# Kernel tuning notes

Measured on AMD Instinct MI355X. Metric: run time of the kernel, lower is better.

The kernel has to match this reference:

```python
import jax, jax.numpy as jnp
import numpy as np

IH, IW = 32, 32
HEADS, DIM_HEAD = 8, 32
EPS = 1e-6


def conv3x3(x, w):
    # x: [B,C,H,W], w: [O,I,3,3], stride 1, pad 1, no bias
    return jax.lax.conv_general_dilated(x, w, (1, 1), ((1, 1), (1, 1)),
                                        dimension_numbers=('NCHW', 'OIHW', 'NCHW'))


def groupnorm1(x, g, b):
    # GroupNorm(1, C): normalize over (C,H,W) per sample
    mu = jnp.mean(x, axis=(1, 2, 3), keepdims=True)
    var = jnp.var(x, axis=(1, 2, 3), keepdims=True)
    xn = (x - mu) * jax.lax.rsqrt(var + EPS)
    return xn * g[None, :, None, None] + b[None, :, None, None]


def proj(x, w, g, b):
    return jax.nn.gelu(groupnorm1(conv3x3(x, w), g, b), approximate=False)


def relative_index(ih, iw):
    coords = np.stack(np.meshgrid(np.arange(ih), np.arange(iw), indexing='ij')).reshape(2, -1)
    rel = coords[:, :, None] - coords[:, None, :]  # [2, n, n]
    rel[0] += ih - 1
    rel[1] += iw - 1
    rel[0] *= 2 * iw - 1
    return jnp.asarray(rel.sum(0).reshape(-1))  # [n*n]


def setup_inputs() -> dict:
    key = jax.random.key(0)
    ks = jax.random.split(key, 9)
    C = HEADS * DIM_HEAD  # 256
    B = 8
    s = 0.02
    inp = {
        'x': jax.random.normal(ks[0], (B, C, IH, IW), jnp.float32),
        'wq': jax.random.normal(ks[1], (C, C, 3, 3), jnp.float32) * s,
        'wk': jax.random.normal(ks[2], (C, C, 3, 3), jnp.float32) * s,
        'wv': jax.random.normal(ks[3], (C, C, 3, 3), jnp.float32) * s,
        'gq': jnp.ones((C,), jnp.float32), 'bq': jnp.zeros((C,), jnp.float32),
        'gk': jnp.ones((C,), jnp.float32), 'bk': jnp.zeros((C,), jnp.float32),
        'gv': jnp.ones((C,), jnp.float32), 'bv': jnp.zeros((C,), jnp.float32),
        'bias_table': jax.random.normal(ks[4], ((2 * IH - 1) * (2 * IW - 1), HEADS), jnp.float32) * s,
        'wo': jax.random.normal(ks[5], (C, C), jnp.float32) * s,
        'bo': jnp.zeros((C,), jnp.float32),
    }
    return inp


def reference(x, wq, wk, wv, gq, bq, gk, bk, gv, bv, bias_table, wo, bo):
    B, C, ih, iw = x.shape
    n = ih * iw
    h, d = HEADS, DIM_HEAD

    q = proj(x, wq, gq, bq)  # [B,C,H,W]
    k = proj(x, wk, gk, bk)
    v = proj(x, wv, gv, bv)

    # 'b c ih iw -> b (ih iw) c' then 'b n (h d) -> b h n d'  ==  [B,h,d,n] -> [B,h,n,d]
    def to_heads(t):
        return t.reshape(B, h, d, n).transpose(0, 1, 3, 2)

    q4, k4, v4 = to_heads(q), to_heads(k), to_heads(v)

    # NOTE: original code applies self.scale only when y is not None; y=None here -> no scale.
    dots = jnp.einsum('bhnd,bhmd->bhnm', q4, k4)  # [B,h,n,n]

    rel_idx = relative_index(ih, iw)  # [n*n]
    rel_bias = bias_table[rel_idx].reshape(n, n, h).transpose(2, 0, 1)[None]  # [1,h,n,n]

    attn = jax.nn.softmax(dots + rel_bias, axis=-1)
    out = jnp.einsum('bhnm,bhmd->bhnd', attn, v4)  # [B,h,n,d]

    # 'b h n d -> b n (h d)' then 'b (ih iw) c -> b c ih iw'
    out = out.transpose(0, 2, 1, 3).reshape(B, n, C).transpose(0, 2, 1).reshape(B, C, ih, iw)

    # to_out: 1x1 conv with bias (dropout=0 in eval)
    out = jnp.einsum('oc,bchw->bohw', wo, out) + bo[None, :, None, None]
    return out
```

## Files before the change

kernel.cpp:

```cpp
#include <hip/hip_runtime.h>
#include <cstdint>
#include <cstddef>

#define GEPS 1e-6f

using bf16x8 = __attribute__((ext_vector_type(8))) short;
using f32x4  = __attribute__((ext_vector_type(4))) float;

__device__ inline ushort f2bf(float x) {
    union { float f; uint32_t u; } v; v.f = x;
    uint32_t r = (v.u + 0x7fffu + ((v.u >> 16) & 1u)) >> 16;
    return (ushort)r;
}
__device__ inline float bf2f(ushort b) {
    union { float f; uint32_t u; } v; v.u = ((uint32_t)b) << 16;
    return v.f;
}

__device__ inline void gll16(const void* g, void* l) {
    __builtin_amdgcn_global_load_lds(
        (const __attribute__((address_space(1))) void*)g,
        (__attribute__((address_space(3))) void*)l, 16, 0, 0);
}

__global__ __launch_bounds__(256) void prep_k(
    const float* __restrict__ x,
    const float* __restrict__ wq, const float* __restrict__ wk,
    const float* __restrict__ wv, const float* __restrict__ wo,
    const float* __restrict__ btab,
    ushort* __restrict__ Ab, ushort* __restrict__ Wbuf,
    ushort* __restrict__ wo_bf, ushort* __restrict__ Bx)
{
    __shared__ __align__(16) ushort Xs[3 * 34 * 128];
    int tid = threadIdx.x;
    int blk = blockIdx.x;

    if (blk < 512) {
        int b = blk >> 6, py = (blk >> 1) & 31, half = blk & 1;
#pragma unroll
        for (int p = tid; p < 768; p += 256) {
            int yy = p >> 8;
            int q = p & 255;
            int col = (q >> 7) ? 33 : 0;
            int ci = q & 127;
            Xs[(yy * 34 + col) * 128 + ci] = 0;
        }
#pragma unroll
        for (int it = 0; it < 12; ++it) {
            int j = it * 256 + tid;
            int ci_l = j / 24;
            int o = (j - ci_l * 24) * 4;
            int yy = o >> 5, xx = o & 31;
            int row = py - 1 + yy;
            float4 v = make_float4(0.f, 0.f, 0.f, 0.f);
            if (row >= 0 && row < 32)
                v = *(const float4*)&x[((size_t)(b * 256 + half * 128 + ci_l)) * 1024 + row * 32 + xx];
            int base = (yy * 34 + xx + 1) * 128 + ci_l;
            Xs[base + 0 * 128] = f2bf(v.x);
            Xs[base + 1 * 128] = f2bf(v.y);
            Xs[base + 2 * 128] = f2bf(v.z);
            Xs[base + 3 * 128] = f2bf(v.w);
        }
        __syncthreads();
        ushort* dst = Ab + (size_t)(b * 1024 + py * 32) * 2304;
#pragma unroll
        for (int it = 0; it < 18; ++it) {
            int idx = it * 256 + tid;
            int ci8l = idx & 15;
            int tp = (idx >> 4) % 9;
            int px = idx / 144;
            int kh = tp / 3, kw = tp - kh * 3;
            uint4 p = *(const uint4*)&Xs[(kh * 34 + px + kw) * 128 + ci8l * 8];
            *(uint4*)&dst[(size_t)(px * 288 + tp * 32 + half * 16 + ci8l) * 8] = p;
        }
        return;
    }
    if (blk < 1280) {
        int wrow = blk - 512;
        int proj = wrow >> 8, co = wrow & 255;
        const float* src = ((proj == 0) ? wq : ((proj == 1) ? wk : wv)) + (size_t)co * 2304;
#pragma unroll
        for (int j = 0; j < 9; ++j) {
            int idx = j * 256 + tid;
            Xs[idx] = f2bf(src[idx]);
        }
        __syncthreads();
        ushort* dst = Wbuf + (size_t)wrow * 2304;
#pragma unroll
        for (int j = 0; j < 9; ++j)
            dst[j * 256 + tid] = Xs[tid * 9 + j];
        return;
    }
    if (blk < 1344) {
        int t = (blk - 1280) * 256 + tid;
        float4 v = *(const float4*)&wo[(size_t)t * 4];
        union { uint2 u; ushort s[4]; } o;
        o.s[0] = f2bf(v.x); o.s[1] = f2bf(v.y); o.s[2] = f2bf(v.z); o.s[3] = f2bf(v.w);
        *(uint2*)&wo_bf[(size_t)t * 4] = o.u;
        return;
    }
    int g = (blk - 1344) * 4 + (tid >> 6);
    int l = tid & 63;
    int h = g >> 10, qt = (g >> 4) & 63, kt = g & 15;
    int quad = l >> 4, c = l & 15;
    union { uint4 v[2]; ushort s[16]; } o;
#pragma unroll
    for (int f = 0; f < 4; ++f)
#pragma unroll
        for (int r = 0; r < 4; ++r) {
            int qrow = qt * 16 + quad * 4 + r;
            int key = kt * 64 + f * 16 + c;
            int dy = (qrow >> 5) - (key >> 5) + 31;
            int dx = (qrow & 31) - (key & 31) + 31;
            o.s[f * 4 + r] = f2bf(btab[(dy * 63 + dx) * 8 + h]);
        }
    uint4* dst = (uint4*)(Bx + ((size_t)g * 64 + l) * 16);
    dst[0] = o.v[0];
    dst[1] = o.v[1];
}

__global__ __launch_bounds__(256, 3) void gemm_bt(
    const ushort* __restrict__ A, const ushort* __restrict__ B,
    int M, int N, int K,
    ushort* __restrict__ Cpart,
    float* __restrict__ Cout, const float* __restrict__ bias, int mode)
{
    __shared__ __align__(16) ushort As[128 * 64];
    __shared__ __align__(16) ushort Bs[128 * 64];
    int tid = threadIdx.x;
    int mbase = blockIdx.x * 128, nbase = blockIdx.y * 128;
    int kspan = K / gridDim.z;
    int k0 = blockIdx.z * kspan;
    int wave = tid >> 6, lane = tid & 63;
    int wm = wave & 1, wn = wave >> 1;
    int quad = lane >> 4, c = lane & 15;

    int row_s = tid >> 3;
    int cc8 = (tid & 7) ^ (row_s & 7);
    ushort* ldsA = As + wave * 512;
    ushort* ldsB = Bs + wave * 512;

    f32x4 acc[4][4];
#pragma unroll
    for (int i = 0; i < 4; ++i)
#pragma unroll
        for (int j = 0; j < 4; ++j) acc[i][j] = (f32x4){0.f, 0.f, 0.f, 0.f};

    for (int kb = k0; kb < k0 + kspan; kb += 64) {
        __syncthreads();
#pragma unroll
        for (int R = 0; R < 4; ++R) {
            int row = R * 32 + row_s;
            gll16(A + (size_t)(mbase + row) * K + kb + cc8 * 8,
                  ldsA + R * 2048);
            gll16(B + (size_t)(nbase + row) * K + kb + cc8 * 8,
                  ldsB + R * 2048);
        }
        __syncthreads();
#pragma unroll
        for (int kq = 0; kq < 2; ++kq) {
            bf16x8 af[4], bfr[4];
            int sw = ((kq * 4 + quad) ^ (c & 7)) * 8;
#pragma unroll
            for (int i = 0; i < 4; ++i) {
                af[i]  = *(const bf16x8*)&As[(wm * 64 + i * 16 + c) * 64 + sw];
                bfr[i] = *(const bf16x8*)&Bs[(wn * 64 + i * 16 + c) * 64 + sw];
            }
#pragma unroll
            for (int i = 0; i < 4; ++i)
#pragma unroll
                for (int j = 0; j < 4; ++j)
                    acc[i][j] = __builtin_amdgcn_mfma_f32_16x16x32_bf16(
                        af[i], bfr[j], acc[i][j], 0, 0, 0);
        }
    }

    if (mode == 0) {
        ushort* Cp = Cpart + (size_t)blockIdx.z * M * N;
#pragma unroll
        for (int i = 0; i < 4; ++i) {
            int mrow = mbase + wm * 64 + i * 16 + quad * 4;
#pragma unroll
            for (int j = 0; j < 4; ++j) {
                int ncol = nbase + wn * 64 + j * 16 + c;
#pragma unroll
                for (int r = 0; r < 4; ++r)
                    Cp[(size_t)(mrow + r) * N + ncol] = f2bf(acc[i][j][r]);
            }
        }
    } else {
#pragma unroll
        for (int i = 0; i < 4; ++i) {
            int mrow0 = mbase + wm * 64 + i * 16 + quad * 4;
#pragma unroll
            for (int j = 0; j < 4; ++j) {
                int ncol = nbase + wn * 64 + j * 16 + c;
                int bb = ncol >> 10, px = ncol & 1023;
#pragma unroll
                for (int r = 0; r < 4; ++r) {
                    int o = mrow0 + r;
                    Cout[((size_t)bb * 256 + o) * 1024 + px] = acc[i][j][r] + bias[o];
                }
            }
        }
    }
}

__global__ __launch_bounds__(256) void stats1_k(const ushort* __restrict__ P0,
                                                const ushort* __restrict__ P1,
                                                float2* __restrict__ part)
{
    int t = blockIdx.x * 256 + threadIdx.x;
    size_t base = (size_t)t * 8;
    union { uint4 v; ushort s[8]; } a, b2;
    a.v  = *(const uint4*)&P0[base];
    b2.v = *(const uint4*)&P1[base];
    float s1 = 0.f, s2 = 0.f;
#pragma unroll
    for (int e = 0; e < 8; ++e) {
        float v = bf2f(a.s[e]) + bf2f(b2.s[e]);
        s1 += v; s2 += v * v;
    }
#pragma unroll
    for (int mk = 1; mk < 32; mk <<= 1) {
        s1 += __shfl_xor(s1, mk, 64);
        s2 += __shfl_xor(s2, mk, 64);
    }
    if ((threadIdx.x & 31) == 0) {
        int gg = t >> 5;
        int m = gg / 3;
        int proj = gg - m * 3;
        int b = m >> 10, slot = m & 1023;
        part[(proj * 8 + b) * 1024 + slot] = make_float2(s1, s2);
    }
}

__global__ __launch_bounds__(256) void stats2_k(const float2* __restrict__ part,
                                                float* __restrict__ stats)
{
    __shared__ float w1[4], w2[4];
    int s = blockIdx.x, tid = threadIdx.x;
    float s1 = 0.f, s2 = 0.f;
#pragma unroll
    for (int i = 0; i < 4; ++i) {
        float2 v = part[(size_t)s * 1024 + tid * 4 + i];
        s1 += v.x; s2 += v.y;
    }
#pragma unroll
    for (int mk = 1; mk < 64; mk <<= 1) {
        s1 += __shfl_xor(s1, mk, 64);
        s2 += __shfl_xor(s2, mk, 64);
    }
    if ((tid & 63) == 0) { w1[tid >> 6] = s1; w2[tid >> 6] = s2; }
    __syncthreads();
    if (tid == 0) {
        stats[s * 2 + 0] = w1[0] + w1[1] + w1[2] + w1[3];
        stats[s * 2 + 1] = w2[0] + w2[1] + w2[2] + w2[3];
    }
}

__global__ void gn_k(const ushort* __restrict__ P0, const ushort* __restrict__ P1,
                     const float* __restrict__ stats,
                     const float* __restrict__ gq, const float* __restrict__ bq,
                     const float* __restrict__ gk, const float* __restrict__ bk,
                     const float* __restrict__ gv, const float* __restrict__ bv,
                     ushort* __restrict__ qb, ushort* __restrict__ kb2,
                     ushort* __restrict__ vx)
{
    int t = blockIdx.x * 256 + threadIdx.x;
    int m = t / 96;
    int nn = (t - m * 96) * 8;
    int proj = nn >> 8, co = nn & 255;
    int b = m >> 10, px = m & 1023;
    float s1 = stats[(proj * 8 + b) * 2 + 0];
    float s2 = stats[(proj * 8 + b) * 2 + 1];
    const float Ninv = 1.f / 262144.f;
    float mu = s1 * Ninv;
    float var = fmaxf(s2 * Ninv - mu * mu, 0.f);
    float rsig = rsqrtf(var + GEPS);
    const float* gam = (proj == 0) ? gq : ((proj == 1) ? gk : gv);
    const float* bet = (proj == 0) ? bq : ((proj == 1) ? bk : bv);

    size_t base = (size_t)m * 768 + nn;
    union { uint4 v; ushort s[8]; } a, c2;
    a.v  = *(const uint4*)&P0[base];
    c2.v = *(const uint4*)&P1[base];
    union { uint4 v; ushort s[8]; } outp;
#pragma unroll
    for (int e = 0; e < 8; ++e) {
        int cc = co + e;
        float xv = bf2f(a.s[e]) + bf2f(c2.s[e]);
        float xn = (xv - mu) * rsig * gam[cc] + bet[cc];
        float ge = 0.5f * xn * (1.f + erff(xn * 0.70710678118654752f));
        outp.s[e] = f2bf(ge);
    }
    int h = co >> 5, d = co & 31;
    if (proj == 0) {
        *(uint4*)(qb + ((((size_t)b * 8 + h) * 1024 + px) * 32 + d)) = outp.v;
    } else if (proj == 1) {
        *(uint4*)(kb2 + ((((size_t)b * 8 + h) * 1024 + px) * 32 + d)) = outp.v;
    } else {
        ushort* vb = vx + ((size_t)b * 8 + h) * 32768;
        int kca = px >> 5, quad = (px >> 3) & 3, j = px & 7;
#pragma unroll
        for (int e = 0; e < 8; ++e) {
            int dd = d + e;
            vb[(((kca * 2 + (dd >> 4)) * 64) + quad * 16 + (dd & 15)) * 8 + j] = outp.s[e];
        }
    }
}

__global__ __launch_bounds__(256, 8) void attn_k(
    const ushort* __restrict__ qb, const ushort* __restrict__ kb,
    const ushort* __restrict__ vx, const ushort* __restrict__ Bx,
    ushort* __restrict__ Opart, float* __restrict__ lpart)
{
    __shared__ __align__(16) ushort Pl[4 * 16 * 72];
    int tid = threadIdx.x, wave = tid >> 6, lane = tid & 63;
    int quad = lane >> 4, c = lane & 15;
    int bh = blockIdx.y;
    int h = bh & 7;
    int z = blockIdx.z;
    int qbase = blockIdx.x * 64 + wave * 16;

    const ushort* Q  = qb + (size_t)bh * 1024 * 32;
    const ushort* Kp = kb + (size_t)bh * 1024 * 32;
    const ushort* Vb = vx + (size_t)bh * 32768;
    const ushort* bxp = Bx + (((size_t)(h * 64 + (qbase >> 4)) * 16) * 64 + lane) * 16;
    ushort* Pw = Pl + wave * 16 * 72;

    bf16x8 qf = *(const bf16x8*)&Q[(qbase + c) * 32 + quad * 8];

    float l_[4] = {0.f, 0.f, 0.f, 0.f};
    f32x4 Of0 = {0.f, 0.f, 0.f, 0.f}, Of1 = {0.f, 0.f, 0.f, 0.f};

    for (int kb64 = z * 512; kb64 < z * 512 + 512; kb64 += 64) {
        f32x4 S[4];
        f32x4 zf = {0.f, 0.f, 0.f, 0.f};
#pragma unroll
        for (int f = 0; f < 4; ++f) {
            bf16x8 kf = *(const bf16x8*)&Kp[(kb64 + f * 16 + c) * 32 + quad * 8];
            S[f] = __builtin_amdgcn_mfma_f32_16x16x32_bf16(qf, kf, zf, 0, 0, 0);
        }
        union { uint4 v[2]; ushort s[16]; } bu;
        const uint4* bsrc = (const uint4*)(bxp + (size_t)(kb64 >> 6) * 1024);
        bu.v[0] = bsrc[0];
        bu.v[1] = bsrc[1];
#pragma unroll
        for (int f = 0; f < 4; ++f)
#pragma unroll
            for (int r = 0; r < 4; ++r) {
                float p = __expf(S[f][r] + bf2f(bu.s[f * 4 + r]));
                S[f][r] = p;
                l_[r] += p;
            }
#pragma unroll
        for (int f = 0; f < 4; ++f)
#pragma unroll
            for (int r = 0; r < 4; ++r)
                Pw[(quad * 4 + r) * 72 + f * 16 + c] = f2bf(S[f][r]);
#pragma unroll
        for (int kc = 0; kc < 2; ++kc) {
            int kca = (kb64 >> 5) + kc;
            bf16x8 pf = *(const bf16x8*)&Pw[c * 72 + kc * 32 + quad * 8];
            bf16x8 vf0 = *(const bf16x8*)&Vb[((kca * 2 + 0) * 64 + lane) * 8];
            Of0 = __builtin_amdgcn_mfma_f32_16x16x32_bf16(pf, vf0, Of0, 0, 0, 0);
            bf16x8 vf1 = *(const bf16x8*)&Vb[((kca * 2 + 1) * 64 + lane) * 8];
            Of1 = __builtin_amdgcn_mfma_f32_16x16x32_bf16(pf, vf1, Of1, 0, 0, 0);
        }
    }
#pragma unroll
    for (int r = 0; r < 4; ++r) {
        float l = l_[r];
        l += __shfl_xor(l, 1, 64);
        l += __shfl_xor(l, 2, 64);
        l += __shfl_xor(l, 4, 64);
        l += __shfl_xor(l, 8, 64);
        int qr = qbase + quad * 4 + r;
        size_t ob = (((size_t)z * 64 + bh) * 1024 + qr) * 32;
        Opart[ob + c]      = f2bf(Of0[r]);
        Opart[ob + 16 + c] = f2bf(Of1[r]);
        if (c == 0) lpart[(size_t)z * 65536 + bh * 1024 + qr] = l;
    }
}

__global__ __launch_bounds__(256) void combine_k(const ushort* __restrict__ Opart,
                                                 const float* __restrict__ lpart,
                                                 ushort* __restrict__ attnout)
{
    int t = blockIdx.x * 256 + threadIdx.x;
    int g = t & 3;
    int qg = t >> 2;
    int bh = qg >> 10, qr = qg & 1023;
    int b = bh >> 3, h = bh & 7;
    size_t ob = ((size_t)qg) * 32 + g * 8;
    union { uint4 v; ushort s[8]; } o0, o1;
    o0.v = *(const uint4*)&Opart[ob];
    o1.v = *(const uint4*)&Opart[(size_t)64 * 1024 * 32 + ob];
    float inv = 1.f / (lpart[qg] + lpart[65536 + qg]);
    union { uint4 u; ushort s[8]; } o;
#pragma unroll
    for (int e = 0; e < 8; ++e)
        o.s[e] = f2bf((bf2f(o0.s[e]) + bf2f(o1.s[e])) * inv);
    *(uint4*)&attnout[(((size_t)b * 1024 + qr) * 256) + h * 32 + g * 8] = o.u;
}

extern "C" void kernel_launch(void* const* d_in, const int* in_sizes, int n_in,
                              void* d_out, int out_size, void* d_ws, size_t ws_size,
                              hipStream_t stream)
{
    const float* x    = (const float*)d_in[0];
    const float* wq   = (const float*)d_in[1];
    const float* wk   = (const float*)d_in[2];
    const float* wv   = (const float*)d_in[3];
    const float* gq   = (const float*)d_in[4];
    const float* bq   = (const float*)d_in[5];
    const float* gk   = (const float*)d_in[6];
    const float* bk   = (const float*)d_in[7];
    const float* gv   = (const float*)d_in[8];
    const float* bv   = (const float*)d_in[9];
    const float* btab = (const float*)d_in[10];
    const float* wo   = (const float*)d_in[11];
    const float* bo   = (const float*)d_in[12];
    float* out = (float*)d_out;

    char* w = (char*)d_ws;
    size_t off = 0;
    auto alloc = [&](size_t bytes) -> char* {
        char* p = w + off;
        off += (bytes + 255) & ~(size_t)255;
        return p;
    };
    ushort* Abuf    = (ushort*)alloc(8192ull * 2304 * 2);
    ushort* Wbuf    = (ushort*)alloc(768ull * 2304 * 2);
    ushort* wo_bf   = (ushort*)alloc(65536ull * 2);
    ushort* Bx      = (ushort*)alloc(8192ull * 64 * 16 * 2);
    ushort* P0      = (ushort*)alloc(8192ull * 768 * 2);
    ushort* P1      = (ushort*)alloc(8192ull * 768 * 2);
    float2* part    = (float2*)alloc(48ull * 1024 * 8);
    float*  stats   = (float*)alloc(384);
    ushort* Opart   = (ushort*)alloc(2ull * 64 * 1024 * 32 * 2);
    float*  lpart   = (float*)alloc(2ull * 64 * 1024 * 4);
    ushort* qb      = (ushort*)Abuf;
    ushort* kb2     = qb  + 8ull * 8 * 1024 * 32;
    ushort* vx      = kb2 + 8ull * 8 * 1024 * 32;
    ushort* attnout = vx  + 8ull * 8 * 32 * 1024;

    prep_k<<<3392, 256, 0, stream>>>(x, wq, wk, wv, wo, btab,
                                     Abuf, Wbuf, wo_bf, Bx);
    gemm_bt<<<dim3(64, 6, 2), 256, 0, stream>>>(Abuf, Wbuf, 8192, 768, 2304,
                                                P0, nullptr, nullptr, 0);
    stats1_k<<<3072, 256, 0, stream>>>(P0, P1, part);
    stats2_k<<<48, 256, 0, stream>>>(part, stats);
    gn_k<<<3072, 256, 0, stream>>>(P0, P1, stats, gq, bq, gk, bk, gv, bv,
                                   qb, kb2, vx);
    attn_k<<<dim3(16, 64, 2), 256, 0, stream>>>(qb, kb2, vx, Bx, Opart, lpart);
    combine_k<<<1024, 256, 0, stream>>>(Opart, lpart, attnout);
    gemm_bt<<<dim3(2, 64, 1), 256, 0, stream>>>(wo_bf, attnout, 256, 8192, 256,
                                                nullptr, out, bo, 1);
}
```

Measured before the change: 221.5 us.

## Replace explicit im2col buffer with implicit-GEMM loads from padded channels-last input

Result: faster. 213.0 us (-3.9%).

```diff
diff --git a/kernel.cpp b/kernel.cpp
--- a/kernel.cpp
+++ b/kernel.cpp
@@ -28,55 +28,52 @@
     const float* __restrict__ wq, const float* __restrict__ wk,
     const float* __restrict__ wv, const float* __restrict__ wo,
     const float* __restrict__ btab,
-    ushort* __restrict__ Ab, ushort* __restrict__ Wbuf,
+    ushort* __restrict__ Xcl, ushort* __restrict__ Wbuf,
     ushort* __restrict__ wo_bf, ushort* __restrict__ Bx)
 {
     __shared__ __align__(16) ushort Xs[3 * 34 * 128];
     int tid = threadIdx.x;
     int blk = blockIdx.x;
 
-    if (blk < 512) {
-        int b = blk >> 6, py = (blk >> 1) & 31, half = blk & 1;
-#pragma unroll
-        for (int p = tid; p < 768; p += 256) {
-            int yy = p >> 8;
-            int q = p & 255;
-            int col = (q >> 7) ? 33 : 0;
-            int ci = q & 127;
-            Xs[(yy * 34 + col) * 128 + ci] = 0;
-        }
-#pragma unroll
-        for (int it = 0; it < 12; ++it) {
-            int j = it * 256 + tid;
-            int ci_l = j / 24;
-            int o = (j - ci_l * 24) * 4;
-            int yy = o >> 5, xx = o & 31;
-            int row = py - 1 + yy;
-            float4 v = make_float4(0.f, 0.f, 0.f, 0.f);
-            if (row >= 0 && row < 32)
-                v = *(const float4*)&x[((size_t)(b * 256 + half * 128 + ci_l)) * 1024 + row * 32 + xx];
-            int base = (yy * 34 + xx + 1) * 128 + ci_l;
-            Xs[base + 0 * 128] = f2bf(v.x);
-            Xs[base + 1 * 128] = f2bf(v.y);
-            Xs[base + 2 * 128] = f2bf(v.z);
-            Xs[base + 3 * 128] = f2bf(v.w);
+    if (blk < 256) {
+        int b = blk >> 5, y = blk & 31;
+#pragma unroll
+        for (int it = 0; it < 8; ++it) {
+            int idx = it * 256 + tid;
+            int ci = idx >> 3, pxg = idx & 7;
+            float4 v = *(const float4*)&x[((size_t)(b * 256 + ci)) * 1024 + y * 32 + pxg * 4];
+            int base = (pxg * 4) * 264 + ci;
+            Xs[base + 0 * 264] = f2bf(v.x);
+            Xs[base + 1 * 264] = f2bf(v.y);
+            Xs[base + 2 * 264] = f2bf(v.z);
+            Xs[base + 3 * 264] = f2bf(v.w);
         }
         __syncthreads();
-        ushort* dst = Ab + (size_t)(b * 1024 + py * 32) * 2304;
-#pragma unroll
-        for (int it = 0; it < 18; ++it) {
+        uint4 z4 = make_uint4(0u, 0u, 0u, 0u);
+        ushort* orow = Xcl + ((size_t)(b * 34) + y + 1) * 34 * 256;
+#pragma unroll
+        for (int it = 0; it < 4; ++it) {
             int idx = it * 256 + tid;
-            int ci8l = idx & 15;
-            int tp = (idx >> 4) % 9;
-            int px = idx / 144;
-            int kh = tp / 3, kw = tp - kh * 3;
-            uint4 p = *(const uint4*)&Xs[(kh * 34 + px + kw) * 128 + ci8l * 8];
-            *(uint4*)&dst[(size_t)(px * 288 + tp * 32 + half * 16 + ci8l) * 8] = p;
+            int px = idx >> 5, ci8 = idx & 31;
+            *(uint4*)&orow[(px + 1) * 256 + ci8 * 8] =
+                *(const uint4*)&Xs[px * 264 + ci8 * 8];
+        }
+        if (tid < 64) {
+            int side = tid >> 5, ci8 = tid & 31;
+            *(uint4*)&orow[side * 33 * 256 + ci8 * 8] = z4;
+        }
+        if (y == 0 || y == 31) {
+            ushort* zrow = Xcl + ((size_t)(b * 34) + (y == 0 ? 0 : 33)) * 34 * 256;
+#pragma unroll
+            for (int it = 0; it < 5; ++it) {
+                int idx = it * 256 + tid;
+                if (idx < 1088) *(uint4*)&zrow[idx * 8] = z4;
+            }
         }
         return;
     }
-    if (blk < 1280) {
-        int wrow = blk - 512;
+    if (blk < 1024) {
+        int wrow = blk - 256;
         int proj = wrow >> 8, co = wrow & 255;
         const float* src = ((proj == 0) ? wq : ((proj == 1) ? wk : wv)) + (size_t)co * 2304;
 #pragma unroll
@@ -91,15 +88,15 @@
             dst[j * 256 + tid] = Xs[tid * 9 + j];
         return;
     }
-    if (blk < 1344) {
-        int t = (blk - 1280) * 256 + tid;
+    if (blk < 1088) {
+        int t = (blk - 1024) * 256 + tid;
         float4 v = *(const float4*)&wo[(size_t)t * 4];
         union { uint2 u; ushort s[4]; } o;
         o.s[0] = f2bf(v.x); o.s[1] = f2bf(v.y); o.s[2] = f2bf(v.z); o.s[3] = f2bf(v.w);
         *(uint2*)&wo_bf[(size_t)t * 4] = o.u;
         return;
     }
-    int g = (blk - 1344) * 4 + (tid >> 6);
+    int g = (blk - 1088) * 4 + (tid >> 6);
     int l = tid & 63;
     int h = g >> 10, qt = (g >> 4) & 63, kt = g & 15;
     int quad = l >> 4, c = l & 15;
@@ -140,6 +137,16 @@
     ushort* ldsA = As + wave * 512;
     ushort* ldsB = Bs + wave * 512;
 
+    int rb[4];
+    if (mode == 0) {
+#pragma unroll
+        for (int R = 0; R < 4; ++R) {
+            int r = mbase + R * 32 + row_s;
+            int b_ = r >> 10, yy = (r >> 5) & 31, xx = r & 31;
+            rb[R] = ((b_ * 34 + yy) * 34 + xx) * 256;
+        }
+    }
+
     f32x4 acc[4][4];
 #pragma unroll
     for (int i = 0; i < 4; ++i)
@@ -148,13 +155,26 @@
 
     for (int kb = k0; kb < k0 + kspan; kb += 64) {
         __syncthreads();
-#pragma unroll
-        for (int R = 0; R < 4; ++R) {
-            int row = R * 32 + row_s;
-            gll16(A + (size_t)(mbase + row) * K + kb + cc8 * 8,
-                  ldsA + R * 2048);
-            gll16(B + (size_t)(nbase + row) * K + kb + cc8 * 8,
-                  ldsB + R * 2048);
+        if (mode == 0) {
+            int tap = kb >> 8;
+            int kh = (tap * 11) >> 5;
+            int kw = tap - kh * 3;
+            int toff = (kh * 34 + kw) * 256 + (kb & 255) + cc8 * 8;
+#pragma unroll
+            for (int R = 0; R < 4; ++R) {
+                gll16(A + rb[R] + toff, ldsA + R * 2048);
+                gll16(B + (size_t)(nbase + R * 32 + row_s) * K + kb + cc8 * 8,
+                      ldsB + R * 2048);
+            }
+        } else {
+#pragma unroll
+            for (int R = 0; R < 4; ++R) {
+                int row = R * 32 + row_s;
+                gll16(A + (size_t)(mbase + row) * K + kb + cc8 * 8,
+                      ldsA + R * 2048);
+                gll16(B + (size_t)(nbase + row) * K + kb + cc8 * 8,
+                      ldsB + R * 2048);
+            }
         }
         __syncthreads();
 #pragma unroll
@@ -431,7 +451,7 @@
         off += (bytes + 255) & ~(size_t)255;
         return p;
     };
-    ushort* Abuf    = (ushort*)alloc(8192ull * 2304 * 2);
+    ushort* Xcl     = (ushort*)alloc(8ull * 34 * 34 * 256 * 2);
     ushort* Wbuf    = (ushort*)alloc(768ull * 2304 * 2);
     ushort* wo_bf   = (ushort*)alloc(65536ull * 2);
     ushort* Bx      = (ushort*)alloc(8192ull * 64 * 16 * 2);
@@ -441,14 +461,14 @@
     float*  stats   = (float*)alloc(384);
     ushort* Opart   = (ushort*)alloc(2ull * 64 * 1024 * 32 * 2);
     float*  lpart   = (float*)alloc(2ull * 64 * 1024 * 4);
-    ushort* qb      = (ushort*)Abuf;
-    ushort* kb2     = qb  + 8ull * 8 * 1024 * 32;
-    ushort* vx      = kb2 + 8ull * 8 * 1024 * 32;
-    ushort* attnout = vx  + 8ull * 8 * 32 * 1024;
-
-    prep_k<<<3392, 256, 0, stream>>>(x, wq, wk, wv, wo, btab,
-                                     Abuf, Wbuf, wo_bf, Bx);
-    gemm_bt<<<dim3(64, 6, 2), 256, 0, stream>>>(Abuf, Wbuf, 8192, 768, 2304,
+    ushort* qb      = (ushort*)alloc(8ull * 8 * 1024 * 32 * 2);
+    ushort* kb2     = (ushort*)alloc(8ull * 8 * 1024 * 32 * 2);
+    ushort* vx      = (ushort*)alloc(8ull * 8 * 32 * 1024 * 2);
+    ushort* attnout = (ushort*)alloc(8ull * 1024 * 256 * 2);
+
+    prep_k<<<3136, 256, 0, stream>>>(x, wq, wk, wv, wo, btab,
+                                     Xcl, Wbuf, wo_bf, Bx);
+    gemm_bt<<<dim3(64, 6, 2), 256, 0, stream>>>(Xcl, Wbuf, 8192, 768, 2304,
                                                 P0, nullptr, nullptr, 0);
     stats1_k<<<3072, 256, 0, stream>>>(P0, P1, part);
     stats2_k<<<48, 256, 0, stream>>>(part, stats);
```
